# Optimization experiments

Hardware: AMD Instinct MI355X
Metric: run time of the kernel (lower is better)

## Reference

```python
import jax, jax.numpy as jnp
import numpy as np

EMBED_DIM = 1024
NUM_HEADS = 16
HEAD_DIM = EMBED_DIM // NUM_HEADS
SPARSITY_LAMBDA = 0.01
B, S = 2, 2048


def setup_inputs() -> dict:
    key = jax.random.key(0)
    ks = jax.random.split(key, 10)
    scale = 0.02
    inp = {
        "x": jax.random.normal(ks[0], (B, S, EMBED_DIM), dtype=jnp.float32),
        "Wq": jax.random.normal(ks[1], (EMBED_DIM, EMBED_DIM), dtype=jnp.float32) * scale,
        "bq": jnp.zeros((EMBED_DIM,), dtype=jnp.float32),
        "Wk": jax.random.normal(ks[2], (EMBED_DIM, EMBED_DIM), dtype=jnp.float32) * scale,
        "bk": jnp.zeros((EMBED_DIM,), dtype=jnp.float32),
        "Wv": jax.random.normal(ks[3], (EMBED_DIM, EMBED_DIM), dtype=jnp.float32) * scale,
        "bv": jnp.zeros((EMBED_DIM,), dtype=jnp.float32),
        "Wo": jax.random.normal(ks[4], (EMBED_DIM, EMBED_DIM), dtype=jnp.float32) * scale,
        "bo": jnp.zeros((EMBED_DIM,), dtype=jnp.float32),
        "z": jax.random.normal(ks[5], (NUM_HEADS,), dtype=jnp.float32),
    }
    return inp


def reference(x, Wq, bq, Wk, bk, Wv, bv, Wo, bo, z):
    # Linear layers (torch Linear: y = x @ W.T + b); W here stored as [out, in]
    def split_heads(t):  # [B,S,E] -> [B,H,S,D]
        return t.reshape(B, S, NUM_HEADS, HEAD_DIM).transpose(0, 2, 1, 3)

    q = split_heads(x @ Wq.T + bq)
    k = split_heads(x @ Wk.T + bk)
    v = split_heads(x @ Wv.T + bv)

    scores = jnp.einsum("bhsd,bhtd->bhst", q, k) / jnp.sqrt(jnp.float32(HEAD_DIM))
    gate = jax.nn.sigmoid(z)  # [H], per-head scalar gate on raw scores
    scores = scores * gate[None, :, None, None]
    probs = jax.nn.softmax(scores, axis=-1)
    ctx = jnp.einsum("bhst,bhtd->bhsd", probs, v)  # [B,H,S,D]
    ctx = ctx.transpose(0, 2, 1, 3).reshape(B, S, EMBED_DIM)
    out = ctx @ Wo.T + bo
    penalty = jnp.sum(jax.nn.sigmoid(z)) * SPARSITY_LAMBDA
    return out, penalty
```

## Files before the change

kernel.cpp:

```cpp
#include <hip/hip_runtime.h>

typedef unsigned short ushort_t;
typedef __bf16 bf16x8 __attribute__((ext_vector_type(8)));
typedef float f32x4 __attribute__((ext_vector_type(4)));
typedef float f32x16 __attribute__((ext_vector_type(16)));
typedef unsigned int u32x2 __attribute__((ext_vector_type(2)));

#define DEVI __device__ __forceinline__

constexpr int Ed = 1024;
constexpr int Hh = 16;
constexpr int Dd = 64;
constexpr int Ss = 2048;
constexpr int Mm = 4096;

constexpr int NX4 = Mm * Ed / 4;
constexpr int NW4 = Ed * Ed / 4;

DEVI ushort_t f2bf(float f) {
    union { float f; unsigned int i; } v; v.f = f;
    unsigned int r = v.i + 0x7fffu + ((v.i >> 16) & 1u);
    return (ushort_t)(r >> 16);
}
DEVI ushort_t f2bf_hi(float f) {
    union { float f; unsigned int i; } v; v.f = f;
    return (ushort_t)(v.i >> 16);
}
DEVI unsigned int fbits(float f) {
    union { float f; unsigned int i; } v; v.f = f;
    return v.i;
}
DEVI float fast_exp2(float x) {
    float r;
    asm("v_exp_f32 %0, %1" : "=v"(r) : "v"(x));
    return r;
}
DEVI unsigned int pkbf(float lo, float hi) {
    return (fbits(hi) & 0xffff0000u) | (fbits(lo) >> 16);
}
DEVI void plswap(unsigned int& a, unsigned int& b) {
#if __has_builtin(__builtin_amdgcn_permlane32_swap)
    u32x2 r = __builtin_amdgcn_permlane32_swap(a, b, false, false);
    a = r[0]; b = r[1];
#else
    asm volatile("v_permlane32_swap_b32 %0, %1" : "+v"(a), "+v"(b));
#endif
}

__global__ __launch_bounds__(256) void cvt_all(
    const float* __restrict__ x,  const float* __restrict__ Wq,
    const float* __restrict__ Wk, const float* __restrict__ Wv,
    const float* __restrict__ Wo,
    ushort_t* __restrict__ xb,  ushort_t* __restrict__ Wqb,
    ushort_t* __restrict__ Wkb, ushort_t* __restrict__ Wvb,
    ushort_t* __restrict__ Wob)
{
    int i = blockIdx.x * 256 + threadIdx.x;
    const float* s; ushort_t* d; int off;
    if (i < NX4)                { s = x;  d = xb;  off = i; }
    else if (i < NX4 + NW4)     { s = Wq; d = Wqb; off = i - NX4; }
    else if (i < NX4 + 2 * NW4) { s = Wk; d = Wkb; off = i - NX4 - NW4; }
    else if (i < NX4 + 3 * NW4) { s = Wv; d = Wvb; off = i - NX4 - 2 * NW4; }
    else                        { s = Wo; d = Wob; off = i - NX4 - 3 * NW4; }
    float4 v = ((const float4*)s)[off];
    ushort4 o; o.x = f2bf(v.x); o.y = f2bf(v.y); o.z = f2bf(v.z); o.w = f2bf(v.w);
    ((ushort4*)d)[off] = o;
}

DEVI void gld16(const void* g, void* l) {
    __builtin_amdgcn_global_load_lds(
        (__attribute__((address_space(1))) void*)(g),
        (__attribute__((address_space(3))) void*)(l), 16, 0, 0);
}

DEVI void gemm_core(const ushort_t* __restrict__ A, const ushort_t* __restrict__ W,
                    ushort_t* As, ushort_t* Bs, int tm, int tn, int K,
                    f32x4 acc[4][4])
{
    const int tid  = threadIdx.x;
    const int w    = tid >> 6;
    const int lane = tid & 63;
    const int quad = lane >> 4;
    const int l15  = lane & 15;
    const int wy   = w >> 1, wx = w & 1;
    const int rowc = lane >> 3;
    const int col8s = (((lane & 7) ^ rowc) * 8);
    const int swq  = l15 & 7;

    for (int k0 = 0; k0 < K; k0 += 64) {
        __syncthreads();
#pragma unroll
        for (int i = 0; i < 4; ++i) {
            int chunk = w * 4 + i;
            int row = chunk * 8 + rowc;
            gld16(A + (size_t)(tm + row) * K + k0 + col8s, (char*)As + chunk * 1024);
            gld16(W + (size_t)(tn + row) * K + k0 + col8s, (char*)Bs + chunk * 1024);
        }
        __syncthreads();
#pragma unroll
        for (int ks = 0; ks < 64; ks += 32) {
            const int k4 = ks >> 3;
            bf16x8 a[4], b[4];
#pragma unroll
            for (int mi = 0; mi < 4; ++mi)
                a[mi] = *(const bf16x8*)&As[(wy * 64 + mi * 16 + l15) * 64
                                            + (((quad + k4) ^ swq) * 8)];
#pragma unroll
            for (int ni = 0; ni < 4; ++ni)
                b[ni] = *(const bf16x8*)&Bs[(wx * 64 + ni * 16 + l15) * 64
                                            + (((quad + k4) ^ swq) * 8)];
#pragma unroll
            for (int mi = 0; mi < 4; ++mi)
#pragma unroll
                for (int ni = 0; ni < 4; ++ni)
                    acc[mi][ni] = __builtin_amdgcn_mfma_f32_16x16x32_bf16(
                        a[mi], b[ni], acc[mi][ni], 0, 0, 0);
        }
    }
}

__global__ __launch_bounds__(256, 3) void qkv_gemm(
    const ushort_t* __restrict__ x,
    const ushort_t* __restrict__ Wq, const float* __restrict__ bq,
    const ushort_t* __restrict__ Wk, const float* __restrict__ bk,
    const ushort_t* __restrict__ Wv, const float* __restrict__ bv,
    const float* __restrict__ z,
    ushort_t* __restrict__ qo, ushort_t* __restrict__ ko, ushort_t* __restrict__ vto)
{
    __shared__ __align__(16) ushort_t As[128 * 64];
    __shared__ __align__(16) ushort_t Bs[128 * 64];
    const ushort_t* W; const float* bias; ushort_t* outp; int vmode;
    if (blockIdx.z == 0)      { W = Wq; bias = bq; outp = qo;  vmode = 0; }
    else if (blockIdx.z == 1) { W = Wk; bias = bk; outp = ko;  vmode = 0; }
    else                      { W = Wv; bias = bv; outp = vto; vmode = 1; }

    const int tm = blockIdx.x * 128, tn = blockIdx.y * 128;
    f32x4 acc[4][4] = {};
    gemm_core(x, W, As, Bs, tm, tn, Ed, acc);

    const int tid = threadIdx.x, w = tid >> 6, lane = tid & 63;
    const int quad = lane >> 4, l15 = lane & 15;
    const int wy = w >> 1, wx = w & 1;
    if (vmode == 0) {
#pragma unroll
        for (int ni = 0; ni < 4; ++ni) {
            int gc = tn + wx * 64 + ni * 16 + l15;
            float bb = bias[gc];
            int h = gc >> 6, d = gc & 63;
            float sc = 1.f;
            if (blockIdx.z == 0)
                sc = (1.f / (1.f + __expf(-z[h]))) * 0.18033688f;
#pragma unroll
            for (int mi = 0; mi < 4; ++mi) {
#pragma unroll
                for (int r = 0; r < 4; ++r) {
                    int gr = tm + wy * 64 + mi * 16 + quad * 4 + r;
                    int b_ = gr >> 11, s_ = gr & 2047;
                    float v = (acc[mi][ni][r] + bb) * sc;
                    outp[((size_t)(b_ * Hh + h) * Ss + s_) * Dd + d] = f2bf_hi(v);
                }
            }
        }
    } else {
#pragma unroll
        for (int ni = 0; ni < 4; ++ni) {
            int gc = tn + wx * 64 + ni * 16 + l15;
            float bb = bias[gc];
            int h = gc >> 6, d = gc & 63;
#pragma unroll
            for (int mi = 0; mi < 4; ++mi) {
                int gr0 = tm + wy * 64 + mi * 16 + quad * 4;
                int b_ = gr0 >> 11, s0 = gr0 & 2047;
                u32x2 pk;
                pk[0] = pkbf(acc[mi][ni][0] + bb, acc[mi][ni][1] + bb);
                pk[1] = pkbf(acc[mi][ni][2] + bb, acc[mi][ni][3] + bb);
                *(u32x2*)&outp[((size_t)(b_ * Hh + h) * Dd + d) * Ss + s0] = pk;
            }
        }
    }
}

__global__ __launch_bounds__(256, 3) void out_gemm(
    const ushort_t* __restrict__ ctx, const ushort_t* __restrict__ Wo,
    const float* __restrict__ bo, const float* __restrict__ z,
    float* __restrict__ out)
{
    __shared__ __align__(16) ushort_t As[128 * 64];
    __shared__ __align__(16) ushort_t Bs[64 * 64];
    const int tm = blockIdx.x * 128, tn = blockIdx.y * 64;

    const int tid  = threadIdx.x;
    const int w    = tid >> 6;
    const int lane = tid & 63;
    const int quad = lane >> 4;
    const int l15  = lane & 15;
    const int wy   = w >> 1, wx = w & 1;
    const int rowc = lane >> 3;
    const int col8s = (((lane & 7) ^ rowc) * 8);
    const int swq  = l15 & 7;

    f32x4 acc[4][2] = {};
    for (int k0 = 0; k0 < Ed; k0 += 64) {
        __syncthreads();
#pragma unroll
        for (int i = 0; i < 4; ++i) {
            int chunk = w * 4 + i;
            int row = chunk * 8 + rowc;
            gld16(ctx + (size_t)(tm + row) * Ed + k0 + col8s, (char*)As + chunk * 1024);
        }
#pragma unroll
        for (int i = 0; i < 2; ++i) {
            int chunk = w * 2 + i;
            int row = chunk * 8 + rowc;
            gld16(Wo + (size_t)(tn + row) * Ed + k0 + col8s, (char*)Bs + chunk * 1024);
        }
        __syncthreads();
#pragma unroll
        for (int ks = 0; ks < 64; ks += 32) {
            const int k4 = ks >> 3;
            bf16x8 a[4], b[2];
#pragma unroll
            for (int mi = 0; mi < 4; ++mi)
                a[mi] = *(const bf16x8*)&As[(wy * 64 + mi * 16 + l15) * 64
                                            + (((quad + k4) ^ swq) * 8)];
#pragma unroll
            for (int ni = 0; ni < 2; ++ni)
                b[ni] = *(const bf16x8*)&Bs[(wx * 32 + ni * 16 + l15) * 64
                                            + (((quad + k4) ^ swq) * 8)];
#pragma unroll
            for (int mi = 0; mi < 4; ++mi)
#pragma unroll
                for (int ni = 0; ni < 2; ++ni)
                    acc[mi][ni] = __builtin_amdgcn_mfma_f32_16x16x32_bf16(
                        a[mi], b[ni], acc[mi][ni], 0, 0, 0);
        }
    }

#pragma unroll
    for (int ni = 0; ni < 2; ++ni) {
        int gc = tn + wx * 32 + ni * 16 + l15;
        float bb = bo[gc];
#pragma unroll
        for (int mi = 0; mi < 4; ++mi)
#pragma unroll
            for (int r = 0; r < 4; ++r) {
                int gr = tm + wy * 64 + mi * 16 + quad * 4 + r;
                out[(size_t)gr * Ed + gc] = acc[mi][ni][r] + bb;
            }
    }

    if (blockIdx.x == 0 && blockIdx.y == 0 && tid == 0) {
        float s = 0.f;
        for (int hh = 0; hh < Hh; ++hh) s += 1.f / (1.f + __expf(-z[hh]));
        out[(size_t)Mm * Ed] = s * 0.01f;
    }
}

__global__ __launch_bounds__(256, 3) void attn(
    const ushort_t* __restrict__ Q, const ushort_t* __restrict__ Kk,
    const ushort_t* __restrict__ Vt, const float* __restrict__ z,
    ushort_t* __restrict__ ctx)
{
    __shared__ __align__(16) ushort_t Ks[2][128 * 64];

    const int tid = threadIdx.x, w = tid >> 6, lane = tid & 63;
    const int hi = lane >> 5, l31 = lane & 31;
    const int lin = blockIdx.x + 16 * blockIdx.y;
    const int qt = lin >> 5;
    const int bh = (lin & 7) * 4 + ((lin >> 3) & 3);
    const int h = bh & (Hh - 1), b_ = bh >> 4;
    const size_t base = (size_t)bh * Ss * Dd;

    const int q0 = qt * 128 + w * 32;
    bf16x8 aQ[4];
#pragma unroll
    for (int i = 0; i < 4; ++i)
        aQ[i] = *(const bf16x8*)&Q[base + (size_t)(q0 + l31) * Dd + i * 16 + hi * 8];

    const int rowc = lane >> 3;
    const int gs   = ((lane & 7) ^ rowc) * 8;
    const ushort_t* kSrc[4];
#pragma unroll
    for (int i = 0; i < 4; ++i)
        kSrc[i] = Kk + base + (size_t)(w * 32 + i * 8 + rowc) * Dd + gs;
    const ushort_t* vBase = Vt + base + (size_t)l31 * Ss + hi * 8;

    f32x16 accO[2] = {};
    float lsum = 0.f;

    const int swq = l31 & 7;

#pragma unroll
    for (int i = 0; i < 4; ++i)
        gld16(kSrc[i], (char*)Ks[0] + (w * 4 + i) * 1024);

    for (int kt = 0; kt < Ss / 128; ++kt) {
        const int cur = kt & 1, nxt = cur ^ 1;
        __syncthreads();

        if (kt + 1 < Ss / 128) {
#pragma unroll
            for (int i = 0; i < 4; ++i)
                gld16(kSrc[i] + (size_t)(kt + 1) * 128 * Dd,
                      (char*)Ks[nxt] + (w * 4 + i) * 1024);
        }

#pragma unroll
        for (int sub = 0; sub < 2; ++sub) {
            f32x16 sT[2] = {};
            __builtin_amdgcn_s_setprio(1);
#pragma unroll
            for (int tt = 0; tt < 2; ++tt) {
                const int T = sub * 2 + tt;
#pragma unroll
                for (int i = 0; i < 4; ++i) {
                    bf16x8 kf = *(const bf16x8*)&Ks[cur][(T * 32 + l31) * 64
                                    + (((2 * i + hi) ^ swq) * 8)];
                    sT[tt] = __builtin_amdgcn_mfma_f32_32x32x16_bf16(kf, aQ[i], sT[tt], 0, 0, 0);
                }
            }
            __builtin_amdgcn_s_setprio(0);

            float p[2][16];
#pragma unroll
            for (int tt = 0; tt < 2; ++tt)
#pragma unroll
                for (int r = 0; r < 16; ++r) {
                    p[tt][r] = fast_exp2(sT[tt][r]);
                    lsum += p[tt][r];
                }

            const int keyb = kt * 128 + sub * 64;
#pragma unroll
            for (int ks = 0; ks < 4; ++ks) {
                const int tt = ks >> 1, h8 = (ks & 1) * 8;
                unsigned int w0 = pkbf(p[tt][h8 + 0], p[tt][h8 + 1]);
                unsigned int w2 = pkbf(p[tt][h8 + 4], p[tt][h8 + 5]);
                plswap(w0, w2);
                unsigned int w1 = pkbf(p[tt][h8 + 2], p[tt][h8 + 3]);
                unsigned int w3 = pkbf(p[tt][h8 + 6], p[tt][h8 + 7]);
                plswap(w1, w3);
                union { unsigned int u[4]; bf16x8 v; } pb;
                pb.u[0] = w0; pb.u[1] = w1; pb.u[2] = w2; pb.u[3] = w3;

                __builtin_amdgcn_s_setprio(1);
#pragma unroll
                for (int dblk = 0; dblk < 2; ++dblk) {
                    bf16x8 vf = *(const bf16x8*)(vBase + (size_t)(dblk * 32) * Ss
                                                 + keyb + ks * 16);
                    accO[dblk] = __builtin_amdgcn_mfma_f32_32x32x16_bf16(vf, pb.v, accO[dblk], 0, 0, 0);
                }
                __builtin_amdgcn_s_setprio(0);
            }
        }
    }

    lsum += __shfl_xor(lsum, 32);
    const float inv = 1.f / lsum;

    ushort_t* crow_p = ctx + ((size_t)(b_ * Ss + q0 + l31)) * Ed + h * Dd;
#pragma unroll
    for (int dblk = 0; dblk < 2; ++dblk)
#pragma unroll
        for (int r = 0; r < 16; r += 2) {
            int d = dblk * 32 + (r & 3) + 8 * (r >> 2) + 4 * hi;
            *(unsigned int*)&crow_p[d] = pkbf(accO[dblk][r] * inv, accO[dblk][r + 1] * inv);
        }
}

extern "C" void kernel_launch(void* const* d_in, const int* in_sizes, int n_in,
                              void* d_out, int out_size, void* d_ws, size_t ws_size,
                              hipStream_t stream) {
    const float* x  = (const float*)d_in[0];
    const float* Wq = (const float*)d_in[1];
    const float* bq = (const float*)d_in[2];
    const float* Wk = (const float*)d_in[3];
    const float* bk = (const float*)d_in[4];
    const float* Wv = (const float*)d_in[5];
    const float* bv = (const float*)d_in[6];
    const float* Wo = (const float*)d_in[7];
    const float* bo = (const float*)d_in[8];
    const float* z  = (const float*)d_in[9];
    float* out = (float*)d_out;

    ushort_t* xb  = (ushort_t*)d_ws;
    ushort_t* Wqb = xb  + (size_t)Mm * Ed;
    ushort_t* Wkb = Wqb + (size_t)Ed * Ed;
    ushort_t* Wvb = Wkb + (size_t)Ed * Ed;
    ushort_t* Wob = Wvb + (size_t)Ed * Ed;
    ushort_t* qw  = Wob + (size_t)Ed * Ed;
    ushort_t* kw  = qw + (size_t)Mm * Ed;
    ushort_t* vT  = kw + (size_t)Mm * Ed;
    ushort_t* cx  = vT + (size_t)Mm * Ed;

    cvt_all<<<dim3((NX4 + 4 * NW4) / 256), dim3(256), 0, stream>>>(
        x, Wq, Wk, Wv, Wo, xb, Wqb, Wkb, Wvb, Wob);
    qkv_gemm<<<dim3(Mm / 128, Ed / 128, 3), dim3(256), 0, stream>>>(
        xb, Wqb, bq, Wkb, bk, Wvb, bv, z, qw, kw, vT);
    attn<<<dim3(Ss / 128, 2 * Hh), dim3(256), 0, stream>>>(qw, kw, vT, z, cx);
    out_gemm<<<dim3(Mm / 128, Ed / 64), dim3(256), 0, stream>>>(cx, Wob, bo, z, out);
}
```

Baseline: 211.7 us.

## Software-pipeline V fragment loads into registers with ping-pong buffers in attention

The attention kernel now prefetches V fragments for the next 64-key half into register double buffers (vfA/vfB) while the current half's QK MFMAs and exp run, instead of loading V from global right before each PV MFMA. The sub loop is manually unrolled into two halves to alternate buffers. This hides global load latency for V but raises register pressure, so launch bounds are lowered from 3 to 2 blocks per SM, which reduces occupancy.

```diff
diff --git a/kernel.cpp b/kernel.cpp
--- a/kernel.cpp
+++ b/kernel.cpp
@@ -256,7 +256,7 @@
     }
 }
 
-__global__ __launch_bounds__(256, 3) void attn(
+__global__ __launch_bounds__(256, 2) void attn(
     const ushort_t* __restrict__ Q, const ushort_t* __restrict__ Kk,
     const ushort_t* __restrict__ Vt, const float* __restrict__ z,
     ushort_t* __restrict__ ctx)
@@ -294,6 +294,13 @@
     for (int i = 0; i < 4; ++i)
         gld16(kSrc[i], (char*)Ks[0] + (w * 4 + i) * 1024);
 
+    bf16x8 vfA[4][2], vfB[4][2];
+#pragma unroll
+    for (int ks = 0; ks < 4; ++ks)
+#pragma unroll
+        for (int dblk = 0; dblk < 2; ++dblk)
+            vfA[ks][dblk] = *(const bf16x8*)(vBase + (size_t)(dblk * 32) * Ss + ks * 16);
+
     for (int kt = 0; kt < Ss / 128; ++kt) {
         const int cur = kt & 1, nxt = cur ^ 1;
         __syncthreads();
@@ -305,21 +312,29 @@
                       (char*)Ks[nxt] + (w * 4 + i) * 1024);
         }
 
-#pragma unroll
-        for (int sub = 0; sub < 2; ++sub) {
+        {
             f32x16 sT[2] = {};
             __builtin_amdgcn_s_setprio(1);
 #pragma unroll
             for (int tt = 0; tt < 2; ++tt) {
-                const int T = sub * 2 + tt;
 #pragma unroll
                 for (int i = 0; i < 4; ++i) {
-                    bf16x8 kf = *(const bf16x8*)&Ks[cur][(T * 32 + l31) * 64
+                    bf16x8 kf = *(const bf16x8*)&Ks[cur][(tt * 32 + l31) * 64
                                     + (((2 * i + hi) ^ swq) * 8)];
                     sT[tt] = __builtin_amdgcn_mfma_f32_32x32x16_bf16(kf, aQ[i], sT[tt], 0, 0, 0);
                 }
             }
             __builtin_amdgcn_s_setprio(0);
+
+            {
+                const int kb = kt * 128 + 64;
+#pragma unroll
+                for (int ks = 0; ks < 4; ++ks)
+#pragma unroll
+                    for (int dblk = 0; dblk < 2; ++dblk)
+                        vfB[ks][dblk] = *(const bf16x8*)(vBase + (size_t)(dblk * 32) * Ss
+                                                         + kb + ks * 16);
+            }
 
             float p[2][16];
 #pragma unroll
@@ -330,7 +345,6 @@
                     lsum += p[tt][r];
                 }
 
-            const int keyb = kt * 128 + sub * 64;
 #pragma unroll
             for (int ks = 0; ks < 4; ++ks) {
                 const int tt = ks >> 1, h8 = (ks & 1) * 8;
@@ -345,11 +359,62 @@
 
                 __builtin_amdgcn_s_setprio(1);
 #pragma unroll
-                for (int dblk = 0; dblk < 2; ++dblk) {
-                    bf16x8 vf = *(const bf16x8*)(vBase + (size_t)(dblk * 32) * Ss
-                                                 + keyb + ks * 16);
-                    accO[dblk] = __builtin_amdgcn_mfma_f32_32x32x16_bf16(vf, pb.v, accO[dblk], 0, 0, 0);
+                for (int dblk = 0; dblk < 2; ++dblk)
+                    accO[dblk] = __builtin_amdgcn_mfma_f32_32x32x16_bf16(
+                        vfA[ks][dblk], pb.v, accO[dblk], 0, 0, 0);
+                __builtin_amdgcn_s_setprio(0);
+            }
+        }
+        {
+            f32x16 sT[2] = {};
+            __builtin_amdgcn_s_setprio(1);
+#pragma unroll
+            for (int tt = 0; tt < 2; ++tt) {
+#pragma unroll
+                for (int i = 0; i < 4; ++i) {
+                    bf16x8 kf = *(const bf16x8*)&Ks[cur][((2 + tt) * 32 + l31) * 64
+                                    + (((2 * i + hi) ^ swq) * 8)];
+                    sT[tt] = __builtin_amdgcn_mfma_f32_32x32x16_bf16(kf, aQ[i], sT[tt], 0, 0, 0);
                 }
+            }
+            __builtin_amdgcn_s_setprio(0);
+
+            if (kt + 1 < Ss / 128) {
+                const int kb = (kt + 1) * 128;
+#pragma unroll
+                for (int ks = 0; ks < 4; ++ks)
+#pragma unroll
+                    for (int dblk = 0; dblk < 2; ++dblk)
+                        vfA[ks][dblk] = *(const bf16x8*)(vBase + (size_t)(dblk * 32) * Ss
+                                                         + kb + ks * 16);
+            }
+
+            float p[2][16];
+#pragma unroll
+            for (int tt = 0; tt < 2; ++tt)
+#pragma unroll
+                for (int r = 0; r < 16; ++r) {
+                    p[tt][r] = fast_exp2(sT[tt][r]);
+                    lsum += p[tt][r];
+                }
+
+#pragma unroll
+            for (int ks = 0; ks < 4; ++ks) {
+                const int tt = ks >> 1, h8 = (ks & 1) * 8;
+                unsigned int w0 = pkbf(p[tt][h8 + 0], p[tt][h8 + 1]);
+                unsigned int w2 = pkbf(p[tt][h8 + 4], p[tt][h8 + 5]);
+                plswap(w0, w2);
+                unsigned int w1 = pkbf(p[tt][h8 + 2], p[tt][h8 + 3]);
+                unsigned int w3 = pkbf(p[tt][h8 + 6], p[tt][h8 + 7]);
+                plswap(w1, w3);
+                union { unsigned int u[4]; bf16x8 v; } pb;
+                pb.u[0] = w0; pb.u[1] = w1; pb.u[2] = w2; pb.u[3] = w3;
+
+                __builtin_amdgcn_s_setprio(1);
+#pragma unroll
+                for (int dblk = 0; dblk < 2; ++dblk)
+                    accO[dblk] = __builtin_amdgcn_mfma_f32_32x32x16_bf16(
+                        vfB[ks][dblk], pb.v, accO[dblk], 0, 0, 0);
                 __builtin_amdgcn_s_setprio(0);
             }
         }
```

Result: slower. 216.6 us (+2.3%).

## Give each wave private K buffers and prefetch V fragments into registers

Applied to the files above, without the earlier changes.

The attention kernel's shared K tile is replaced by per-wave private double buffers of 64 keys. Each wave loads its own K copy, so the block-wide __syncthreads is dropped. V fragments are now prefetched into registers one tile ahead, and manual vmcnt waits overlap the next loads with the current MFMA work. The cost is four times the K global and LDS traffic, more registers and LDS per block, and a lower occupancy hint (launch bounds 2 instead of 3). The vmcnt(16) count also depends on the exact number of loads issued.

```diff
diff --git a/kernel.cpp b/kernel.cpp
--- a/kernel.cpp
+++ b/kernel.cpp
@@ -256,12 +256,12 @@
     }
 }
 
-__global__ __launch_bounds__(256, 3) void attn(
+__global__ __launch_bounds__(256, 2) void attn(
     const ushort_t* __restrict__ Q, const ushort_t* __restrict__ Kk,
     const ushort_t* __restrict__ Vt, const float* __restrict__ z,
     ushort_t* __restrict__ ctx)
 {
-    __shared__ __align__(16) ushort_t Ks[2][128 * 64];
+    __shared__ __align__(16) ushort_t Ks[4][2][64 * 64];
 
     const int tid = threadIdx.x, w = tid >> 6, lane = tid & 63;
     const int hi = lane >> 5, l31 = lane & 31;
@@ -279,79 +279,104 @@
 
     const int rowc = lane >> 3;
     const int gs   = ((lane & 7) ^ rowc) * 8;
-    const ushort_t* kSrc[4];
-#pragma unroll
-    for (int i = 0; i < 4; ++i)
-        kSrc[i] = Kk + base + (size_t)(w * 32 + i * 8 + rowc) * Dd + gs;
+    const ushort_t* kSrcBase = Kk + base + (size_t)rowc * Dd + gs;
+    ushort_t* myKs0 = &Ks[w][0][0];
+    ushort_t* myKs1 = &Ks[w][1][0];
     const ushort_t* vBase = Vt + base + (size_t)l31 * Ss + hi * 8;
 
     f32x16 accO[2] = {};
     float lsum = 0.f;
-
     const int swq = l31 & 7;
 
-#pragma unroll
-    for (int i = 0; i < 4; ++i)
-        gld16(kSrc[i], (char*)Ks[0] + (w * 4 + i) * 1024);
-
-    for (int kt = 0; kt < Ss / 128; ++kt) {
-        const int cur = kt & 1, nxt = cur ^ 1;
-        __syncthreads();
-
-        if (kt + 1 < Ss / 128) {
-#pragma unroll
-            for (int i = 0; i < 4; ++i)
-                gld16(kSrc[i] + (size_t)(kt + 1) * 128 * Dd,
-                      (char*)Ks[nxt] + (w * 4 + i) * 1024);
-        }
-
-#pragma unroll
-        for (int sub = 0; sub < 2; ++sub) {
-            f32x16 sT[2] = {};
+    bf16x8 vfA[4][2], vfB[4][2];
+
+    auto TILE = [&](const ushort_t* kbuf, bf16x8 (&vf)[4][2]) {
+        f32x16 sT[2] = {};
+        __builtin_amdgcn_s_setprio(1);
+#pragma unroll
+        for (int tt = 0; tt < 2; ++tt)
+#pragma unroll
+            for (int i = 0; i < 4; ++i) {
+                bf16x8 kf = *(const bf16x8*)&kbuf[(tt * 32 + l31) * 64
+                                + (((2 * i + hi) ^ swq) * 8)];
+                sT[tt] = __builtin_amdgcn_mfma_f32_32x32x16_bf16(kf, aQ[i], sT[tt], 0, 0, 0);
+            }
+        __builtin_amdgcn_s_setprio(0);
+
+        float p[2][16];
+#pragma unroll
+        for (int tt = 0; tt < 2; ++tt)
+#pragma unroll
+            for (int r = 0; r < 16; ++r) {
+                p[tt][r] = fast_exp2(sT[tt][r]);
+                lsum += p[tt][r];
+            }
+
+#pragma unroll
+        for (int ks = 0; ks < 4; ++ks) {
+            const int tt = ks >> 1, h8 = (ks & 1) * 8;
+            unsigned int w0 = pkbf(p[tt][h8 + 0], p[tt][h8 + 1]);
+            unsigned int w2 = pkbf(p[tt][h8 + 4], p[tt][h8 + 5]);
+            plswap(w0, w2);
+            unsigned int w1 = pkbf(p[tt][h8 + 2], p[tt][h8 + 3]);
+            unsigned int w3 = pkbf(p[tt][h8 + 6], p[tt][h8 + 7]);
+            plswap(w1, w3);
+            union { unsigned int u[4]; bf16x8 v; } pb;
+            pb.u[0] = w0; pb.u[1] = w1; pb.u[2] = w2; pb.u[3] = w3;
+
             __builtin_amdgcn_s_setprio(1);
 #pragma unroll
-            for (int tt = 0; tt < 2; ++tt) {
-                const int T = sub * 2 + tt;
-#pragma unroll
-                for (int i = 0; i < 4; ++i) {
-                    bf16x8 kf = *(const bf16x8*)&Ks[cur][(T * 32 + l31) * 64
-                                    + (((2 * i + hi) ^ swq) * 8)];
-                    sT[tt] = __builtin_amdgcn_mfma_f32_32x32x16_bf16(kf, aQ[i], sT[tt], 0, 0, 0);
-                }
-            }
+            for (int dblk = 0; dblk < 2; ++dblk)
+                accO[dblk] = __builtin_amdgcn_mfma_f32_32x32x16_bf16(
+                    vf[ks][dblk], pb.v, accO[dblk], 0, 0, 0);
             __builtin_amdgcn_s_setprio(0);
-
-            float p[2][16];
-#pragma unroll
-            for (int tt = 0; tt < 2; ++tt)
-#pragma unroll
-                for (int r = 0; r < 16; ++r) {
-                    p[tt][r] = fast_exp2(sT[tt][r]);
-                    lsum += p[tt][r];
-                }
-
-            const int keyb = kt * 128 + sub * 64;
-#pragma unroll
-            for (int ks = 0; ks < 4; ++ks) {
-                const int tt = ks >> 1, h8 = (ks & 1) * 8;
-                unsigned int w0 = pkbf(p[tt][h8 + 0], p[tt][h8 + 1]);
-                unsigned int w2 = pkbf(p[tt][h8 + 4], p[tt][h8 + 5]);
-                plswap(w0, w2);
-                unsigned int w1 = pkbf(p[tt][h8 + 2], p[tt][h8 + 3]);
-                unsigned int w3 = pkbf(p[tt][h8 + 6], p[tt][h8 + 7]);
-                plswap(w1, w3);
-                union { unsigned int u[4]; bf16x8 v; } pb;
-                pb.u[0] = w0; pb.u[1] = w1; pb.u[2] = w2; pb.u[3] = w3;
-
-                __builtin_amdgcn_s_setprio(1);
-#pragma unroll
-                for (int dblk = 0; dblk < 2; ++dblk) {
-                    bf16x8 vf = *(const bf16x8*)(vBase + (size_t)(dblk * 32) * Ss
-                                                 + keyb + ks * 16);
-                    accO[dblk] = __builtin_amdgcn_mfma_f32_32x32x16_bf16(vf, pb.v, accO[dblk], 0, 0, 0);
-                }
-                __builtin_amdgcn_s_setprio(0);
-            }
+        }
+    };
+
+#pragma unroll
+    for (int ks = 0; ks < 4; ++ks)
+#pragma unroll
+        for (int dblk = 0; dblk < 2; ++dblk)
+            vfA[ks][dblk] = *(const bf16x8*)(vBase + (size_t)(dblk * 32) * Ss + ks * 16);
+#pragma unroll
+    for (int c = 0; c < 8; ++c)
+        gld16(kSrcBase + (size_t)(c * 8) * Dd, (char*)myKs0 + c * 1024);
+
+    constexpr int NT = Ss / 64;
+    for (int t = 0; t < NT; t += 2) {
+        {
+            const int kb = (t + 1) * 64;
+#pragma unroll
+            for (int ks = 0; ks < 4; ++ks)
+#pragma unroll
+                for (int dblk = 0; dblk < 2; ++dblk)
+                    vfB[ks][dblk] = *(const bf16x8*)(vBase + (size_t)(dblk * 32) * Ss
+                                                     + kb + ks * 16);
+#pragma unroll
+            for (int c = 0; c < 8; ++c)
+                gld16(kSrcBase + (size_t)(kb + c * 8) * Dd, (char*)myKs1 + c * 1024);
+            asm volatile("s_waitcnt vmcnt(16)" ::: "memory");
+            __builtin_amdgcn_sched_barrier(0);
+            TILE(myKs0, vfA);
+        }
+        {
+            if (t + 2 < NT) {
+                const int kb = (t + 2) * 64;
+#pragma unroll
+                for (int ks = 0; ks < 4; ++ks)
+#pragma unroll
+                    for (int dblk = 0; dblk < 2; ++dblk)
+                        vfA[ks][dblk] = *(const bf16x8*)(vBase + (size_t)(dblk * 32) * Ss
+                                                         + kb + ks * 16);
+#pragma unroll
+                for (int c = 0; c < 8; ++c)
+                    gld16(kSrcBase + (size_t)(kb + c * 8) * Dd, (char*)myKs0 + c * 1024);
+                asm volatile("s_waitcnt vmcnt(16)" ::: "memory");
+            } else {
+                asm volatile("s_waitcnt vmcnt(0)" ::: "memory");
+            }
+            __builtin_amdgcn_sched_barrier(0);
+            TILE(myKs1, vfB);
         }
     }
 
```

Result: slower. 224.8 us (+6.2%).
